# Performance work log

Hardware: AMD Instinct MI355X
Metric: run time of the kernel (lower is better)

## Reference

```python
import jax, jax.numpy as jnp
import numpy as np
from jax import lax

BN_EPS = 1e-5


def setup_inputs() -> dict:
    key = jax.random.key(0)
    ks = jax.random.split(key, 4)
    B, C1, H, W = 16, 256, 64, 64
    E, C2, K = 4, 256, 3
    x = jax.random.normal(ks[0], (B, C1, H, W), dtype=jnp.float32)
    w_route = jax.random.normal(ks[1], (E, C1), dtype=jnp.float32) * 0.02
    b_route = jnp.zeros((E,), dtype=jnp.float32)
    w_experts = jax.random.normal(ks[2], (E, C2, C1, K, K), dtype=jnp.float32) * 0.02
    bn_gamma = jnp.ones((C2,), dtype=jnp.float32)
    bn_beta = jnp.zeros((C2,), dtype=jnp.float32)
    bn_mean = jnp.zeros((C2,), dtype=jnp.float32)
    bn_var = jnp.ones((C2,), dtype=jnp.float32)
    return {"x": x, "w_route": w_route, "b_route": b_route,
            "w_experts": w_experts, "bn_gamma": bn_gamma, "bn_beta": bn_beta,
            "bn_mean": bn_mean, "bn_var": bn_var}


def reference(x, w_route, b_route, w_experts, bn_gamma, bn_beta, bn_mean, bn_var):
    # Routing: global average pool -> linear -> sigmoid. [B, E]
    pooled = jnp.mean(x, axis=(2, 3))
    routing = jax.nn.sigmoid(pooled @ w_route.T + b_route)

    # All num_experts conv passes in one grouped-output conv (same math as the
    # per-expert loop in the original): stack expert filters along out-channels.
    E, Co, Ci, kh, kw = w_experts.shape
    w = w_experts.reshape(E * Co, Ci, kh, kw)
    pad = kh // 2  # autopad(3) = 1
    y = lax.conv_general_dilated(
        x, w, window_strides=(1, 1), padding=[(pad, pad), (pad, pad)],
        dimension_numbers=("NCHW", "OIHW", "NCHW"))  # [B, E*Co, H, W]
    B, _, Ho, Wo = y.shape
    y = y.reshape(B, E, Co, Ho, Wo)

    # Per-sample weighted sum over experts.
    out = jnp.einsum("beohw,be->bohw", y, routing)

    # BatchNorm2d (inference form: running stats) + SiLU.
    inv = bn_gamma / jnp.sqrt(bn_var + BN_EPS)
    out = out * inv[None, :, None, None] + (bn_beta - bn_mean * inv)[None, :, None, None]
    return jax.nn.silu(out)
```

## Files before the change

kernel.cpp:

```cpp
#include <hip/hip_runtime.h>
#include <stdint.h>

typedef unsigned int uint;
typedef unsigned short ushort;
typedef __attribute__((ext_vector_type(8))) short short8;
typedef __attribute__((ext_vector_type(4))) float f32x4;

__device__ float  g_pooled[16 * 256];
__device__ ushort g_wct[16 * 9 * 256 * 256];
__device__ ushort g_xt[16 * 64 * 64 * 256];
__device__ ushort g_zero[8];
__device__ uint   g_isf32;

__device__ __forceinline__ float bf2f(ushort u) {
    return __uint_as_float(((uint)u) << 16);
}
__device__ __forceinline__ ushort f2bf(float f) {
    uint u = __float_as_uint(f);
    return (ushort)((u + 0x7fffu + ((u >> 16) & 1u)) >> 16);
}

__global__ void detect_zero_kernel(const uint* __restrict__ bn_g_u) {
    int t = threadIdx.x;
    for (int i = t; i < 16 * 256; i += 256) g_pooled[i] = 0.f;
    if (t < 8) g_zero[t] = 0;
    if (t == 0) g_isf32 = (bn_g_u[0] == 0x3F800000u) ? 1u : 0u;
}

__global__ __launch_bounds__(256) void xt_pool_kernel(const void* __restrict__ xraw) {
    __shared__ float tf[64 * 65];
    uint* tile = (uint*)tf;
    const int c0 = blockIdx.x * 64, h = blockIdx.y, b = blockIdx.z;
    const int t = threadIdx.x;
    uint* xtu = (uint*)g_xt;
    const uint isf32 = g_isf32;
    if (isf32) {
        const float* xf = (const float*)xraw;
#pragma unroll
        for (int p = 0; p < 16; ++p) {
            int idx = p * 256 + t;
            int cil = idx >> 6, w = idx & 63;
            tf[cil * 65 + w] = xf[(((size_t)(b * 256 + c0 + cil)) * 64 + h) * 64 + w];
        }
        __syncthreads();
#pragma unroll
        for (int p = 0; p < 8; ++p) {
            int w = p * 8 + (t >> 5), cid = t & 31;
            uint lo = f2bf(tf[(2 * cid) * 65 + w]);
            uint hi = f2bf(tf[(2 * cid + 1) * 65 + w]);
            xtu[(((size_t)b * 64 + h) * 64 + w) * 128 + (c0 >> 1) + cid] = lo | (hi << 16);
        }
        if (t < 64) {
            float s = 0.f;
#pragma unroll
            for (int w = 0; w < 64; ++w) s += tf[t * 65 + w];
            atomicAdd(&g_pooled[b * 256 + c0 + t], s);
        }
    } else {
        const uint* xu = (const uint*)xraw;
#pragma unroll
        for (int p = 0; p < 8; ++p) {
            int cil = p * 8 + (t >> 5), wd = t & 31;
            tile[cil * 33 + wd] =
                xu[(((size_t)(b * 256 + c0 + cil)) * 64 + h) * 32 + wd];
        }
        __syncthreads();
#pragma unroll
        for (int p = 0; p < 8; ++p) {
            int w = p * 8 + (t >> 5), cid = t & 31;
            uint a = tile[(2 * cid) * 33 + (w >> 1)];
            uint bb = tile[(2 * cid + 1) * 33 + (w >> 1)];
            uint lo = (w & 1) ? (a >> 16) : (a & 0xffffu);
            uint hi = (w & 1) ? (bb >> 16) : (bb & 0xffffu);
            xtu[(((size_t)b * 64 + h) * 64 + w) * 128 + (c0 >> 1) + cid] = lo | (hi << 16);
        }
        if (t < 64) {
            float s = 0.f;
#pragma unroll
            for (int wd = 0; wd < 32; ++wd) {
                uint u = tile[t * 33 + wd];
                s += __uint_as_float(u << 16) + __uint_as_float(u & 0xffff0000u);
            }
            atomicAdd(&g_pooled[b * 256 + c0 + t], s);
        }
    }
}

__global__ __launch_bounds__(256) void wcomb_kernel(const void* __restrict__ w_exp,
                                                    const void* __restrict__ w_route,
                                                    const void* __restrict__ b_route) {
    __shared__ float s_rout[64];
    const int co = blockIdx.x, ci = threadIdx.x;
    const uint isf32 = g_isf32;
    if (ci < 64) {
        int b = ci >> 2, e = ci & 3;
        float s;
        if (isf32) {
            const float* wr = (const float*)w_route;
            s = ((const float*)b_route)[e];
            for (int c = 0; c < 256; ++c)
                s += g_pooled[b * 256 + c] * (1.f / 4096.f) * wr[e * 256 + c];
        } else {
            const ushort* wr = (const ushort*)w_route;
            s = bf2f(((const ushort*)b_route)[e]);
            for (int c = 0; c < 256; ++c)
                s += g_pooled[b * 256 + c] * (1.f / 4096.f) * bf2f(wr[e * 256 + c]);
        }
        s_rout[ci] = 1.f / (1.f + __expf(-s));
    }
    float we[4][9];
    if (isf32) {
        const float* wf = (const float*)w_exp;
#pragma unroll
        for (int e = 0; e < 4; ++e) {
            const float* p = wf + (((size_t)e * 256 + co) * 256 + ci) * 9;
#pragma unroll
            for (int tp = 0; tp < 9; ++tp) we[e][tp] = p[tp];
        }
    } else {
        const ushort* wb = (const ushort*)w_exp;
#pragma unroll
        for (int e = 0; e < 4; ++e) {
            const ushort* p = wb + (((size_t)e * 256 + co) * 256 + ci) * 9;
#pragma unroll
            for (int tp = 0; tp < 9; ++tp) we[e][tp] = bf2f(p[tp]);
        }
    }
    __syncthreads();
    for (int b = 0; b < 16; ++b) {
        float r0 = s_rout[b * 4 + 0], r1 = s_rout[b * 4 + 1];
        float r2 = s_rout[b * 4 + 2], r3 = s_rout[b * 4 + 3];
#pragma unroll
        for (int tp = 0; tp < 9; ++tp) {
            float a = r0 * we[0][tp] + r1 * we[1][tp] + r2 * we[2][tp] + r3 * we[3][tp];
            g_wct[(((size_t)b * 9 + tp) * 256 + co) * 256 + ci] = f2bf(a);
        }
    }
}

#define LDS_SWZ(o) ((o) ^ (((o) >> 3) & 0x30))

__device__ __forceinline__ void stage_iter(int it, int t, int wave, int h0,
                                           const ushort* __restrict__ wct_p,
                                           const ushort* __restrict__ xt_p,
                                           ushort* s_w, ushort* s_x) {
    const int cc = it / 3, kh = it - cc * 3;
    const int ci0 = cc * 32;
#pragma unroll
    for (int i = 0; i < 6; ++i) {
        int p = i * 4096 + t * 16;
        int f = LDS_SWZ(p);
        int kw = f >> 13;
        int rem = f & 8191;
        int col = rem >> 6;
        int cio = (rem & 63) >> 1;
        const ushort* src = wct_p +
            (((size_t)(kh * 3 + kw) * 256 + col) * 256 + ci0 + cio);
        char* dst = (char*)s_w + i * 4096 + wave * 1024;
        __builtin_amdgcn_global_load_lds(
            (const __attribute__((address_space(1))) void*)src,
            (__attribute__((address_space(3))) void*)dst, 16, 0, 0);
    }
#pragma unroll
    for (int i = 0; i < 2; ++i) {
        int phys = i * 4224 + 64 + t * 16;
        int o = LDS_SWZ(phys);
        int rem2 = o - (i * 4224 + 64);
        int col = rem2 >> 6;
        int cio = (rem2 & 63) >> 1;
        int h_in = h0 + kh - 1 + i;
        const ushort* src = (h_in >= 0 && h_in < 64)
            ? xt_p + (((size_t)h_in * 64 + col) * 256 + ci0 + cio)
            : g_zero;
        char* dst = (char*)s_x + i * 4224 + 64 + wave * 1024;
        __builtin_amdgcn_global_load_lds(
            (const __attribute__((address_space(1))) void*)src,
            (__attribute__((address_space(3))) void*)dst, 16, 0, 0);
    }
}

__global__ __launch_bounds__(256) void conv_kernel(
    const void* __restrict__ bn_g, const void* __restrict__ bn_b,
    const void* __restrict__ bn_m, const void* __restrict__ bn_v,
    void* __restrict__ outv) {
    __shared__ __align__(16) ushort s_x[2 * 66 * 32];
    __shared__ __align__(16) ushort s_w[3 * 128 * 32];
    __shared__ float bn_inv[128], bn_add[128];

    const int t = threadIdx.x;
    const int lane = t & 63;
    const int q = lane >> 4, l16 = lane & 15;
    const int wave = __builtin_amdgcn_readfirstlane(t >> 6);
    const int u = blockIdx.x;
    const int pair = u & 31, hw = u >> 5;
    const int b = pair >> 1;
    const int co0 = (pair & 1) * 128;
    const int h0 = hw * 2;
    const int wm = wave & 1, wn = wave >> 1;
    const uint isf32 = g_isf32;

    if (t < 128) {
        int co = co0 + t;
        float g, be, mn, vr;
        if (isf32) {
            g = ((const float*)bn_g)[co]; be = ((const float*)bn_b)[co];
            mn = ((const float*)bn_m)[co]; vr = ((const float*)bn_v)[co];
        } else {
            g = bf2f(((const ushort*)bn_g)[co]); be = bf2f(((const ushort*)bn_b)[co]);
            mn = bf2f(((const ushort*)bn_m)[co]); vr = bf2f(((const ushort*)bn_v)[co]);
        }
        float inv = g * __frsqrt_rn(vr + 1e-5f);
        bn_inv[t] = inv;
        bn_add[t] = be - mn * inv;
        int r = t >> 6, side = (t >> 5) & 1, ci = t & 31;
        s_x[(r * 66 + side * 65) * 32 + ci] = 0;
    }

    f32x4 acc[4][4];
#pragma unroll
    for (int mt = 0; mt < 4; ++mt)
#pragma unroll
        for (int nt = 0; nt < 4; ++nt) acc[mt][nt] = (f32x4){0.f, 0.f, 0.f, 0.f};

    const ushort* xt_p  = g_xt  + (size_t)b * 64 * 64 * 256;
    const ushort* wct_p = g_wct + (size_t)b * 9 * 256 * 256 + (size_t)co0 * 256;

    stage_iter(0, t, wave, h0, wct_p, xt_p, s_w, s_x);

    for (int it = 0; it < 24; ++it) {
        __syncthreads();
#pragma unroll
        for (int kw = 0; kw < 3; ++kw) {
            short8 a[4], bf[4];
#pragma unroll
            for (int mt = 0; mt < 4; ++mt) {
                int o = ((kw * 128 + wm * 64 + mt * 16 + l16) * 32 + q * 8) * 2;
                a[mt] = *(const short8*)((const char*)s_w + LDS_SWZ(o));
            }
#pragma unroll
            for (int nt = 0; nt < 4; ++nt) {
                int o = ((wn * 66 + nt * 16 + l16 + kw) * 32 + q * 8) * 2;
                bf[nt] = *(const short8*)((const char*)s_x + LDS_SWZ(o));
            }
#pragma unroll
            for (int mt = 0; mt < 4; ++mt)
#pragma unroll
                for (int nt = 0; nt < 4; ++nt)
                    acc[mt][nt] = __builtin_amdgcn_mfma_f32_16x16x32_bf16(
                        a[mt], bf[nt], acc[mt][nt], 0, 0, 0);
        }
        __syncthreads();
        if (it + 1 < 24)
            stage_iter(it + 1, t, wave, h0, wct_p, xt_p, s_w, s_x);
    }

#pragma unroll
    for (int mt = 0; mt < 4; ++mt) {
        int co_l = wm * 64 + mt * 16 + q * 4;
#pragma unroll
        for (int i = 0; i < 4; ++i) {
            float inv = bn_inv[co_l + i], add = bn_add[co_l + i];
            int co = co0 + co_l + i;
#pragma unroll
            for (int nt = 0; nt < 4; ++nt) {
                int n_local = wn * 64 + nt * 16 + l16;
                int h = h0 + (n_local >> 6), w = n_local & 63;
                float v = acc[mt][nt][i] * inv + add;
                float s = v / (1.f + __expf(-v));
                size_t idx = (((size_t)b * 256 + co) * 64 + h) * 64 + w;
                if (isf32) ((float*)outv)[idx] = s;
                else       ((ushort*)outv)[idx] = f2bf(s);
            }
        }
    }
}

extern "C" void kernel_launch(void* const* d_in, const int* in_sizes, int n_in,
                              void* d_out, int out_size, void* d_ws, size_t ws_size,
                              hipStream_t stream) {
    const void* x       = d_in[0];
    const void* w_route = d_in[1];
    const void* b_route = d_in[2];
    const void* w_exp   = d_in[3];
    const void* bn_g    = d_in[4];
    const void* bn_b    = d_in[5];
    const void* bn_m    = d_in[6];
    const void* bn_v    = d_in[7];
    (void)d_ws; (void)ws_size;

    detect_zero_kernel<<<1, 256, 0, stream>>>((const uint*)bn_g);
    xt_pool_kernel<<<dim3(4, 64, 16), 256, 0, stream>>>(x);
    wcomb_kernel<<<256, 256, 0, stream>>>(w_exp, w_route, b_route);
    conv_kernel<<<1024, 256, 0, stream>>>(bn_g, bn_b, bn_m, bn_v, d_out);
}
```

Before: 258.6 us.

## Double-buffer LDS tiles to overlap global-to-LDS loads with MFMA compute

Splits the shared-memory weight and input tiles into two buffers. The next iteration's global_load_lds is issued into the alternate buffer before the current buffer's MFMAs run, with explicit vmcnt waits and raw barriers replacing the paired __syncthreads. The goal is to hide global load latency behind matrix compute. It doubles LDS use, which may reduce occupancy, and the correctness of the manual waitcnt depends on how many loads stage_iter issues.

Result: no change. 263.5 us (+1.9%).

```diff
diff --git a/kernel.cpp b/kernel.cpp
--- a/kernel.cpp
+++ b/kernel.cpp
@@ -183,8 +183,8 @@
     const void* __restrict__ bn_g, const void* __restrict__ bn_b,
     const void* __restrict__ bn_m, const void* __restrict__ bn_v,
     void* __restrict__ outv) {
-    __shared__ __align__(16) ushort s_x[2 * 66 * 32];
-    __shared__ __align__(16) ushort s_w[3 * 128 * 32];
+    __shared__ __align__(16) ushort s_x[2][2 * 66 * 32];
+    __shared__ __align__(16) ushort s_w[2][3 * 128 * 32];
     __shared__ float bn_inv[128], bn_add[128];
 
     const int t = threadIdx.x;
@@ -213,7 +213,8 @@
         bn_inv[t] = inv;
         bn_add[t] = be - mn * inv;
         int r = t >> 6, side = (t >> 5) & 1, ci = t & 31;
-        s_x[(r * 66 + side * 65) * 32 + ci] = 0;
+        s_x[0][(r * 66 + side * 65) * 32 + ci] = 0;
+        s_x[1][(r * 66 + side * 65) * 32 + ci] = 0;
     }
 
     f32x4 acc[4][4];
@@ -225,22 +226,33 @@
     const ushort* xt_p  = g_xt  + (size_t)b * 64 * 64 * 256;
     const ushort* wct_p = g_wct + (size_t)b * 9 * 256 * 256 + (size_t)co0 * 256;
 
-    stage_iter(0, t, wave, h0, wct_p, xt_p, s_w, s_x);
+    stage_iter(0, t, wave, h0, wct_p, xt_p, (ushort*)s_w[0], (ushort*)s_x[0]);
+    asm volatile("s_waitcnt lgkmcnt(0)" ::: "memory");
 
     for (int it = 0; it < 24; ++it) {
-        __syncthreads();
+        const int cur = it & 1;
+        if (it + 1 < 24) {
+            stage_iter(it + 1, t, wave, h0, wct_p, xt_p,
+                       (ushort*)s_w[cur ^ 1], (ushort*)s_x[cur ^ 1]);
+            asm volatile("s_waitcnt vmcnt(8)" ::: "memory");
+        } else {
+            asm volatile("s_waitcnt vmcnt(0)" ::: "memory");
+        }
+        __builtin_amdgcn_s_barrier();
+        const ushort* sw = s_w[cur];
+        const ushort* sx = s_x[cur];
 #pragma unroll
         for (int kw = 0; kw < 3; ++kw) {
             short8 a[4], bf[4];
 #pragma unroll
             for (int mt = 0; mt < 4; ++mt) {
                 int o = ((kw * 128 + wm * 64 + mt * 16 + l16) * 32 + q * 8) * 2;
-                a[mt] = *(const short8*)((const char*)s_w + LDS_SWZ(o));
+                a[mt] = *(const short8*)((const char*)sw + LDS_SWZ(o));
             }
 #pragma unroll
             for (int nt = 0; nt < 4; ++nt) {
                 int o = ((wn * 66 + nt * 16 + l16 + kw) * 32 + q * 8) * 2;
-                bf[nt] = *(const short8*)((const char*)s_x + LDS_SWZ(o));
+                bf[nt] = *(const short8*)((const char*)sx + LDS_SWZ(o));
             }
 #pragma unroll
             for (int mt = 0; mt < 4; ++mt)
@@ -249,9 +261,8 @@
                     acc[mt][nt] = __builtin_amdgcn_mfma_f32_16x16x32_bf16(
                         a[mt], bf[nt], acc[mt][nt], 0, 0, 0);
         }
-        __syncthreads();
-        if (it + 1 < 24)
-            stage_iter(it + 1, t, wave, h0, wct_p, xt_p, s_w, s_x);
+        asm volatile("s_waitcnt lgkmcnt(0)" ::: "memory");
+        __builtin_amdgcn_s_barrier();
     }
 
 #pragma unroll
```
